# Optimization experiments

Measured on AMD Instinct MI355X. Metric: run time of the kernel, lower is better.

The kernel has to match this reference:

```python
import jax, jax.numpy as jnp
import numpy as np

B, N_PER, DEG = 1024, 256, 16
N = B * N_PER            # 262144 total nodes
E = B * N_PER * DEG      # 4194304 edges
F_IN, H, K, C = 7, 64, 50, 2


def setup_inputs() -> dict:
    key = jax.random.key(0)
    ks = jax.random.split(key, 16)
    rng = np.random.default_rng(0)
    # within-graph random edges: nodes of graph g occupy [g*N_PER, (g+1)*N_PER)
    offs = np.repeat(np.arange(B, dtype=np.int64) * N_PER, N_PER * DEG)
    src = offs + rng.integers(0, N_PER, size=E)
    dst = offs + rng.integers(0, N_PER, size=E)
    edge_index = jnp.asarray(np.stack([src, dst]), dtype=jnp.int64)
    batch = jnp.repeat(jnp.arange(B, dtype=jnp.int64), N_PER)
    sc = lambda fan: 1.0 / np.sqrt(fan)
    return {
        'x': jax.random.normal(ks[0], (N, F_IN), jnp.float32),
        'W1a': jax.random.normal(ks[1], (F_IN, H), jnp.float32) * sc(F_IN),
        'b1a': jnp.zeros((H,), jnp.float32),
        'W1b': jax.random.normal(ks[2], (H, H), jnp.float32) * sc(H),
        'b1b': jnp.zeros((H,), jnp.float32),
        'Wp': jax.random.normal(ks[3], (H, K), jnp.float32) * sc(H),
        'bp': jnp.zeros((K,), jnp.float32),
        'W2a': jax.random.normal(ks[4], (H, H), jnp.float32) * sc(H),
        'b2a': jnp.zeros((H,), jnp.float32),
        'W2b': jax.random.normal(ks[5], (H, H), jnp.float32) * sc(H),
        'b2b': jnp.zeros((H,), jnp.float32),
        'Wl': jax.random.normal(ks[6], (H, C), jnp.float32) * sc(H),
        'bl': jnp.zeros((C,), jnp.float32),
        'edge_index': edge_index,
        'batch': batch,
    }


def reference(x, W1a, b1a, W1b, b1b, Wp, bp, W2a, b2a, W2b, b2b, Wl, bl,
              edge_index, batch):
    src, dst = edge_index[0], edge_index[1]
    # --- sparse GINConv (eps=0): MLP(x + sum_{j in N(i)} x_j) ---
    agg = jnp.zeros_like(x).at[dst].add(x[src])          # scatter-add over edges
    h = jax.nn.relu((x + agg) @ W1a + b1a) @ W1b + b1b   # [N, H]
    # --- densify per graph (equal-size contiguous graphs) ---
    xd = h.reshape(B, N_PER, H)                          # [B, n, H]
    g = src // N_PER
    si = src % N_PER
    di = dst % N_PER
    A = jnp.zeros((B, N_PER, N_PER), x.dtype).at[g, si, di].add(1.0)
    # --- BNPool-style soft cluster pooling ---
    S = jax.nn.softmax(xd @ Wp + bp, axis=-1)            # [B, n, K]
    xp = jnp.einsum('bnk,bnd->bkd', S, xd)               # [B, K, H]
    AS = jnp.einsum('bnm,bmk->bnk', A, S)
    Ap = jnp.einsum('bnk,bnl->bkl', S, AS)               # [B, K, K]
    SSt = jnp.einsum('bnk,bmk->bnm', S, S)
    link_loss = jnp.sqrt(jnp.sum((A - SSt) ** 2)) / A.size
    ent_loss = -jnp.mean(jnp.sum(S * jnp.log(S + 1e-15), axis=-1))
    aux_loss = link_loss + ent_loss
    # --- DenseGINConv (eps=0): MLP(x + A @ x) ---
    h2 = xp + jnp.einsum('bkl,bld->bkd', Ap, xp)
    h2 = jax.nn.relu(h2 @ W2a + b2a) @ W2b + b2b         # [B, K, H]
    # --- mean pool over clusters + classifier ---
    logits = h2.mean(axis=1) @ Wl + bl                   # [B, C]
    return jax.nn.log_softmax(logits, axis=-1), aux_loss
```

## Files before the change

kernel.cpp:

```cpp
#include <hip/hip_runtime.h>
#include <math.h>

#define NG   1024
#define NP   256
#define EPG  4096
#define ETOT 4194304
#define FIN  7
#define HD   64
#define KC   50
#define FST  72
#define TST  264
#define TSC  0.00390625f
#define TSCI 256.0f

#define SW_ST(k, n)  ((k) * 256 + ((n) ^ (((k) & 7) << 3)))
#define SW_AW(r, w)  ((r) * 128 + ((w) ^ (((r) & 7) << 2)))
#define SW_AH(r, h)  ((r) * 256 + ((h) ^ (((r) & 7) << 3)))


typedef __attribute__((ext_vector_type(8))) _Float16 v8h;
typedef __attribute__((ext_vector_type(4))) float v4f;

__device__ __align__(16) _Float16 g_W1bT[HD * HD];
__device__ __align__(16) _Float16 g_WWT[HD * HD];
__device__ __align__(16) _Float16 g_W2aT[HD * HD];
__device__ __align__(16) _Float16 g_W2bT[HD * HD];
__device__ float g_bP[HD];

__global__ void kw_conv(const float* __restrict__ W1b, const float* __restrict__ Wp,
                        const float* __restrict__ W2a, const float* __restrict__ W2b,
                        const float* __restrict__ b1b, const float* __restrict__ bp,
                        float* __restrict__ ws) {
    const int b = blockIdx.x, tid = threadIdx.x;
    if (b == 0 && tid < 4) ws[tid] = 0.f;
    {
        int i = b * 256 + tid;
        int d = i >> 6, j = i & 63;
        g_W1bT[i] = (_Float16)W1b[j * HD + d];
        g_W2aT[i] = (_Float16)W2a[j * HD + d];
        g_W2bT[i] = (_Float16)W2b[j * HD + d];
    }
    {
        int k = b * 4 + (tid >> 6), j = tid & 63;
        float acc = 0.f;
        if (k < KC) {
            for (int d = 0; d < HD; ++d)
                acc += W1b[j * HD + d] * Wp[d * KC + k];
        }
        g_WWT[k * HD + j] = (_Float16)acc;
    }
    if (tid < 4) {
        int k = b * 4 + tid;
        float a = 0.f;
        if (k < KC) {
            for (int d = 0; d < HD; ++d) a += b1b[d] * Wp[d * KC + k];
            a += bp[k];
        }
        g_bP[k] = a;
    }
}

__global__ void finalize_k(const float* __restrict__ ws, float* __restrict__ out) {
    if (threadIdx.x == 0) {
        float num = ws[0] - 2.f * ws[2] + ws[3];
        float link = sqrtf(fmaxf(num, 0.f)) / 67108864.0f;
        float ent  = -ws[1] / 262144.0f;
        out[2048] = link + ent;
    }
}

__device__ __forceinline__ float blockReduceN(float v, float* red, int nw) {
    __syncthreads();
    #pragma unroll
    for (int o = 32; o > 0; o >>= 1) v += __shfl_down(v, o);
    if ((threadIdx.x & 63) == 0) red[threadIdx.x >> 6] = v;
    __syncthreads();
    float r = 0.f;
    if (threadIdx.x == 0) {
        for (int i = 0; i < nw; ++i) r += red[i];
    }
    return r;
}

__device__ __forceinline__ void blockReduce3(float& a, float& b, float& c,
                                             float* red) {
    __syncthreads();
    #pragma unroll
    for (int o = 32; o > 0; o >>= 1) {
        a += __shfl_down(a, o);
        b += __shfl_down(b, o);
        c += __shfl_down(c, o);
    }
    const int wid = threadIdx.x >> 6;
    if ((threadIdx.x & 63) == 0) {
        red[wid * 3] = a; red[wid * 3 + 1] = b; red[wid * 3 + 2] = c;
    }
    __syncthreads();
    if (threadIdx.x == 0) {
        float ra = 0.f, rb = 0.f, rc = 0.f;
        for (int i = 0; i < 16; ++i) {
            ra += red[i * 3]; rb += red[i * 3 + 1]; rc += red[i * 3 + 2];
        }
        a = ra; b = rb; c = rc;
    }
}

__launch_bounds__(1024, 1)
__global__ void mega(const int* __restrict__ esrc, const int* __restrict__ edst,
                     const float* __restrict__ x,
                     const float* __restrict__ W1a, const float* __restrict__ b1a,
                     const float* __restrict__ b1b,
                     const float* __restrict__ b2a, const float* __restrict__ b2b,
                     const float* __restrict__ Wl,  const float* __restrict__ bl,
                     float* __restrict__ out, float* __restrict__ ws)
{
    __shared__ __align__(16) _Float16 ST[64 * 256];
    __shared__ __align__(16) _Float16 xagg[NP * 8];
    __shared__ __align__(16) union {
        struct {
            unsigned char ssi[EPG];
            float xt8[NP * 8];
            unsigned int hist[256], cur[256], roff[NP + 1];
        } k1;
        struct {
            _Float16 t1b[NP * FST];
            _Float16 t1T[HD * TST];
        } k2;
        struct {
            unsigned int cnt[64 * 128];
            _Float16 T1T[64 * FST];
        } a;
        struct {
            _Float16 Apf_tf[64 * FST];
            _Float16 xpT[64 * FST];
            _Float16 h2f[64 * FST];
        } b;
    } u;
    __shared__ float cs[64];
    __shared__ float red[48];

    const int g = blockIdx.x, tid = threadIdx.x;
    const int lane = tid & 63, wid = tid >> 6;
    const int l15 = lane & 15, quad = lane >> 4, fko = quad * 8;
    const int mt = (wid >> 2) << 4, nt = (wid & 3) << 4;

    for (int i = tid; i < 64 * 128; i += 1024) ((unsigned int*)ST)[i] = 0u;
    if (tid < 256) u.k1.hist[tid] = 0u;
    __syncthreads();

    unsigned int cellr[4];
    #pragma unroll
    for (int j = 0; j < 4; ++j) {
        int e = tid + j * 1024;
        int s = esrc[g * EPG + e] & (NP - 1);
        int d = edst[g * EPG + e] & (NP - 1);
        cellr[j] = (unsigned)((s << 8) | d);
        atomicAdd(&u.k1.hist[d], 1u);
    }
    for (int i = tid; i < NP * 8; i += 1024) {
        int n = i >> 3, f = i & 7;
        u.k1.xt8[i] = (f < FIN) ? x[g * NP * FIN + n * FIN + f] : 0.f;
    }
    __syncthreads();

    if (wid == 0) {
        unsigned carry = 0;
        for (int c = 0; c < 4; ++c) {
            unsigned v = u.k1.hist[c * 64 + lane];
            unsigned s = v;
            #pragma unroll
            for (int o = 1; o < 64; o <<= 1) {
                unsigned t = __shfl_up(s, o);
                if (lane >= o) s += t;
            }
            unsigned excl = s - v + carry;
            u.k1.roff[c * 64 + lane] = excl;
            u.k1.cur[c * 64 + lane] = excl;
            carry += __shfl(s, 63);
        }
        if (lane == 0) u.k1.roff[NP] = EPG;
    }
    __syncthreads();

    #pragma unroll
    for (int j = 0; j < 4; ++j) {
        unsigned c = cellr[j];
        unsigned p2 = atomicAdd(&u.k1.cur[c & 255u], 1u);
        u.k1.ssi[p2] = (unsigned char)(c >> 8);
    }
    __syncthreads();

    {
        const int gi = tid >> 3, f = tid & 7;
        for (int n = gi; n < NP; n += 128) {
            int beg = u.k1.roff[n], end = u.k1.roff[n + 1];
            float a = u.k1.xt8[n * 8 + f];
            for (int e = beg; e < end; ++e)
                a += u.k1.xt8[u.k1.ssi[e] * 8 + f];
            xagg[n * 8 + f] = (_Float16)a;
        }
    }
    __syncthreads();

    {
        float w1r[FIN];
        #pragma unroll
        for (int f = 0; f < FIN; ++f) w1r[f] = W1a[f * HD + lane];
        float b1r = b1a[lane];
        for (int it = 0; it < 16; ++it) {
            int n = it * 16 + wid;
            float a = b1r;
            #pragma unroll
            for (int f = 0; f < FIN; ++f)
                a += (float)xagg[n * 8 + f] * w1r[f];
            _Float16 tv = (_Float16)fmaxf(a, 0.f);
            u.k2.t1b[n * FST + lane] = tv;
            u.k2.t1T[lane * TST + n] = tv;
        }
    }
    __syncthreads();

    float entL = 0.f;
    {
        const int r16 = wid << 4;
        v4f pa[4];
        #pragma unroll
        for (int c = 0; c < 4; ++c) {
            v4f acc = {0.f, 0.f, 0.f, 0.f};
            #pragma unroll
            for (int ks = 0; ks < 2; ++ks) {
                v8h af = *(const v8h*)&u.k2.t1b[(r16 + l15) * FST + ks * 32 + fko];
                v8h bf = *(const v8h*)&g_WWT[(c * 16 + l15) * HD + ks * 32 + fko];
                acc = __builtin_amdgcn_mfma_f32_16x16x32_f16(af, bf, acc, 0, 0, 0);
            }
            pa[c] = acc;
        }
        float bv[4]; bool valid[4];
        #pragma unroll
        for (int c = 0; c < 4; ++c) {
            int col = c * 16 + l15;
            bv[c] = g_bP[col];
            valid[c] = col < KC;
        }
        #pragma unroll
        for (int r = 0; r < 4; ++r) {
            float pv[4];
            #pragma unroll
            for (int c = 0; c < 4; ++c)
                pv[c] = valid[c] ? (pa[c][r] + bv[c]) : -INFINITY;
            float m = fmaxf(fmaxf(pv[0], pv[1]), fmaxf(pv[2], pv[3]));
            #pragma unroll
            for (int o = 8; o > 0; o >>= 1) m = fmaxf(m, __shfl_xor(m, o));
            float e[4], Z = 0.f;
            #pragma unroll
            for (int c = 0; c < 4; ++c) {
                e[c] = valid[c] ? __expf(pv[c] - m) : 0.f;
                Z += e[c];
            }
            #pragma unroll
            for (int o = 8; o > 0; o >>= 1) Z += __shfl_xor(Z, o);
            float zi = 1.f / Z, lZ = __logf(Z);
            int row = r16 + quad * 4 + r;
            #pragma unroll
            for (int c = 0; c < 4; ++c) {
                if (valid[c]) {
                    float s = e[c] * zi;
                    ST[SW_ST(c * 16 + l15, row)] = (_Float16)s;
                    entL += s * (pv[c] - m);
                }
            }
            if (l15 == 0) entL -= lZ;
        }
    }
    __syncthreads();

    v4f spa = {0.f, 0.f, 0.f, 0.f};
    {
        const int ar = mt + l15, br = nt + l15;
        #pragma unroll
        for (int ks = 0; ks < 8; ++ks) {
            int ko = ks * 32 + fko;
            v8h af = *(const v8h*)&ST[SW_ST(ar, ko)];
            v8h bf = *(const v8h*)&u.k2.t1T[br * TST + ko];
            spa = __builtin_amdgcn_mfma_f32_16x16x32_f16(af, bf, spa, 0, 0, 0);
        }
    }
    {
        _Float16* SPb = u.k2.t1b;
        int c = nt + l15;
        #pragma unroll
        for (int r = 0; r < 4; ++r)
            SPb[(mt + quad * 4 + r) * FST + c] = (_Float16)spa[r];
    }
    {
        int k = tid >> 4, q = tid & 15;
        float v = 0.f;
        #pragma unroll
        for (int i = 0; i < 16; ++i) v += (float)ST[SW_ST(k, q * 16 + i)];
        #pragma unroll
        for (int o = 8; o > 0; o >>= 1) v += __shfl_xor(v, o);
        if (q == 0) cs[k] = v;
    }
    {
        float rE = blockReduceN(entL, red, 16);
        if (tid == 0) atomicAdd(&ws[1], rE);
    }

    v4f axp;
    {
        const int d = nt + l15;
        float bv = b1b[d];
        #pragma unroll
        for (int r = 0; r < 4; ++r) axp[r] = cs[mt + quad * 4 + r] * bv;
        #pragma unroll
        for (int ks = 0; ks < 2; ++ks) {
            v8h af = *(const v8h*)&u.k2.t1b[(mt + l15) * FST + ks * 32 + fko];
            v8h bf = *(const v8h*)&g_W1bT[(nt + l15) * HD + ks * 32 + fko];
            axp = __builtin_amdgcn_mfma_f32_16x16x32_f16(af, bf, axp, 0, 0, 0);
        }
    }
    __syncthreads();

    float sumA2 = 0.f;
    v4f ap = {0.f, 0.f, 0.f, 0.f};
    v4f ag = {0.f, 0.f, 0.f, 0.f};

    for (int ch = 0; ch < 4; ++ch) {
        for (int i = tid; i < 64 * 128; i += 1024) u.a.cnt[i] = 0u;
        __syncthreads();

        int rlo = ch << 6;
        #pragma unroll
        for (int j = 0; j < 4; ++j) {
            unsigned c = cellr[j];
            int sr = (int)(c >> 8) - rlo;
            if ((unsigned)sr < 64u) {
                int d = c & 255u;
                atomicAdd(&u.a.cnt[SW_AW(sr, d >> 1)],
                          (d & 1) ? 0x10000u : 1u);
            }
        }
        __syncthreads();

        for (int i = tid; i < 64 * 128; i += 1024) {
            unsigned v = u.a.cnt[i];
            float m0 = (float)(v & 0xffffu), m1 = (float)(v >> 16);
            sumA2 += m0 * m0 + m1 * m1;
            union { unsigned uu; _Float16 h[2]; } cv;
            cv.h[0] = (_Float16)m0; cv.h[1] = (_Float16)m1;
            u.a.cnt[i] = cv.uu;
        }
        __syncthreads();

        const _Float16* Af = (const _Float16*)u.a.cnt;

        {
            const int ar = mt + l15, br = nt + l15;
            v4f acc = {0.f, 0.f, 0.f, 0.f};
            #pragma unroll
            for (int ks = 0; ks < 8; ++ks) {
                v8h af = *(const v8h*)&Af[SW_AH(ar, ks * 32 + fko)];
                v8h bf = *(const v8h*)&ST[SW_ST(br, ks * 32 + fko)];
                acc = __builtin_amdgcn_mfma_f32_16x16x32_f16(af, bf, acc, 0, 0, 0);
            }
            int c = nt + l15;
            #pragma unroll
            for (int r = 0; r < 4; ++r)
                u.a.T1T[c * FST + mt + quad * 4 + r] = (_Float16)acc[r];
        }
        __syncthreads();

        {
            const int ar = mt + l15, br = nt + l15;
            #pragma unroll
            for (int ks = 0; ks < 2; ++ks) {
                int ko = (ch << 6) + ks * 32 + fko;
                v8h af = *(const v8h*)&ST[SW_ST(ar, ko)];
                v8h bt = *(const v8h*)&u.a.T1T[br * FST + ks * 32 + fko];
                v8h bs = *(const v8h*)&ST[SW_ST(br, ko)];
                ap = __builtin_amdgcn_mfma_f32_16x16x32_f16(af, bt, ap, 0, 0, 0);
                ag = __builtin_amdgcn_mfma_f32_16x16x32_f16(af, bs, ag, 0, 0, 0);
            }
        }
        __syncthreads();
    }

    float tr = 0.f, g2 = 0.f;
    {
        int c = nt + l15;
        #pragma unroll
        for (int r = 0; r < 4; ++r) {
            int k = mt + quad * 4 + r;
            u.b.Apf_tf[k * FST + c] = (_Float16)ap[r];
            u.b.xpT[c * FST + k] = (_Float16)axp[r];
            if (k < KC && c < KC) {
                if (k == c) tr += ap[r];
                g2 += ag[r] * ag[r];
            }
        }
    }

    blockReduce3(sumA2, tr, g2, red);
    if (tid == 0) {
        atomicAdd(&ws[0], sumA2);
        atomicAdd(&ws[2], tr);
        atomicAdd(&ws[3], g2);
    }
    __syncthreads();

    {
        v4f hacc = axp;
        #pragma unroll
        for (int ks = 0; ks < 2; ++ks) {
            v8h af = *(const v8h*)&u.b.Apf_tf[(mt + l15) * FST + ks * 32 + fko];
            v8h bf = *(const v8h*)&u.b.xpT[(nt + l15) * FST + ks * 32 + fko];
            hacc = __builtin_amdgcn_mfma_f32_16x16x32_f16(af, bf, hacc, 0, 0, 0);
        }
        int d = nt + l15;
        #pragma unroll
        for (int r = 0; r < 4; ++r)
            u.b.h2f[(mt + quad * 4 + r) * FST + d] = (_Float16)(hacc[r] * TSC);
    }
    __syncthreads();

    {
        float bv = b2a[nt + l15] * TSC;
        v4f tacc = {bv, bv, bv, bv};
        #pragma unroll
        for (int ks = 0; ks < 2; ++ks) {
            v8h af = *(const v8h*)&u.b.h2f[(mt + l15) * FST + ks * 32 + fko];
            v8h bf = *(const v8h*)&g_W2aT[(nt + l15) * 64 + ks * 32 + fko];
            tacc = __builtin_amdgcn_mfma_f32_16x16x32_f16(af, bf, tacc, 0, 0, 0);
        }
        int d2 = nt + l15;
        #pragma unroll
        for (int r = 0; r < 4; ++r)
            u.b.Apf_tf[(mt + quad * 4 + r) * FST + d2] = (_Float16)fmaxf(tacc[r], 0.f);
    }
    __syncthreads();

    float l0 = 0.f, l1 = 0.f;
    {
        v4f oacc = {0.f, 0.f, 0.f, 0.f};
        #pragma unroll
        for (int ks = 0; ks < 2; ++ks) {
            v8h af = *(const v8h*)&u.b.Apf_tf[(mt + l15) * FST + ks * 32 + fko];
            v8h bf = *(const v8h*)&g_W2bT[(nt + l15) * 64 + ks * 32 + fko];
            oacc = __builtin_amdgcn_mfma_f32_16x16x32_f16(af, bf, oacc, 0, 0, 0);
        }
        int j = nt + l15;
        float bv = b2b[j];
        float wl0 = Wl[j * 2], wl1 = Wl[j * 2 + 1];
        #pragma unroll
        for (int r = 0; r < 4; ++r) {
            int k = mt + quad * 4 + r;
            if (k < KC) {
                float h3v = oacc[r] * TSCI + bv;
                l0 += h3v * wl0; l1 += h3v * wl1;
            }
        }
    }

    float dummy = 0.f;
    blockReduce3(l0, l1, dummy, red);
    if (tid == 0) {
        float g0 = bl[0] + l0 * (1.f / KC);
        float g1 = bl[1] + l1 * (1.f / KC);
        float mm = fmaxf(g0, g1);
        float lse = mm + logf(expf(g0 - mm) + expf(g1 - mm));
        out[2 * g]     = g0 - lse;
        out[2 * g + 1] = g1 - lse;
    }
}

extern "C" void kernel_launch(void* const* d_in, const int* in_sizes, int n_in,
                              void* d_out, int out_size, void* d_ws, size_t ws_size,
                              hipStream_t stream) {
    const float* x    = (const float*)d_in[0];
    const float* W1a  = (const float*)d_in[1];
    const float* b1a  = (const float*)d_in[2];
    const float* W1b  = (const float*)d_in[3];
    const float* b1b  = (const float*)d_in[4];
    const float* Wp   = (const float*)d_in[5];
    const float* bp   = (const float*)d_in[6];
    const float* W2a  = (const float*)d_in[7];
    const float* b2a  = (const float*)d_in[8];
    const float* W2b  = (const float*)d_in[9];
    const float* b2b  = (const float*)d_in[10];
    const float* Wl   = (const float*)d_in[11];
    const float* bl   = (const float*)d_in[12];
    const int*   eidx = (const int*)d_in[13];
    float* out = (float*)d_out;
    float* ws  = (float*)d_ws;

    kw_conv<<<16, 256, 0, stream>>>(W1b, Wp, W2a, W2b, b1b, bp, ws);
    mega<<<NG, 1024, 0, stream>>>(eidx, eidx + ETOT, x,
                                  W1a, b1a, b1b,
                                  b2a, b2b, Wl, bl, out, ws);
    finalize_k<<<1, 64, 0, stream>>>(ws, out);
}
```

Measured before the change: 254.8 us.

## Halve block size and shrink shared memory to fit multiple blocks per CU

The fused per-graph kernel moves from 1024 to 512 threads per block with launch bounds allowing 4 blocks per CU. Shared-memory footprint is reduced by processing the node MLP in two 128-node halves, dropping the transposed t1 buffer, and halving the adjacency count tile so the A·S product runs in 8 chunks of 32 rows. Each wave now owns two output tiles, and the entropy reduction is merged into the final block reduction. The intent is higher occupancy and overlap across graphs, at the cost of more chunks, extra barriers and more register pressure per thread.

```diff
diff --git a/kernel.cpp b/kernel.cpp
--- a/kernel.cpp
+++ b/kernel.cpp
@@ -9,7 +9,7 @@
 #define HD   64
 #define KC   50
 #define FST  72
-#define TST  264
+#define FT2  68
 #define TSC  0.00390625f
 #define TSCI 256.0f
 
@@ -29,10 +29,8 @@
 
 __global__ void kw_conv(const float* __restrict__ W1b, const float* __restrict__ Wp,
                         const float* __restrict__ W2a, const float* __restrict__ W2b,
-                        const float* __restrict__ b1b, const float* __restrict__ bp,
-                        float* __restrict__ ws) {
+                        const float* __restrict__ b1b, const float* __restrict__ bp) {
     const int b = blockIdx.x, tid = threadIdx.x;
-    if (b == 0 && tid < 4) ws[tid] = 0.f;
     {
         int i = b * 256 + tid;
         int d = i >> 6, j = i & 63;
@@ -69,21 +67,8 @@
     }
 }
 
-__device__ __forceinline__ float blockReduceN(float v, float* red, int nw) {
-    __syncthreads();
-    #pragma unroll
-    for (int o = 32; o > 0; o >>= 1) v += __shfl_down(v, o);
-    if ((threadIdx.x & 63) == 0) red[threadIdx.x >> 6] = v;
-    __syncthreads();
-    float r = 0.f;
-    if (threadIdx.x == 0) {
-        for (int i = 0; i < nw; ++i) r += red[i];
-    }
-    return r;
-}
-
-__device__ __forceinline__ void blockReduce3(float& a, float& b, float& c,
-                                             float* red) {
+__device__ __forceinline__ void blockReduce3w8(float& a, float& b, float& c,
+                                               float* red) {
     __syncthreads();
     #pragma unroll
     for (int o = 32; o > 0; o >>= 1) {
@@ -98,14 +83,14 @@
     __syncthreads();
     if (threadIdx.x == 0) {
         float ra = 0.f, rb = 0.f, rc = 0.f;
-        for (int i = 0; i < 16; ++i) {
+        for (int i = 0; i < 8; ++i) {
             ra += red[i * 3]; rb += red[i * 3 + 1]; rc += red[i * 3 + 2];
         }
         a = ra; b = rb; c = rc;
     }
 }
 
-__launch_bounds__(1024, 1)
+__launch_bounds__(512, 4)
 __global__ void mega(const int* __restrict__ esrc, const int* __restrict__ edst,
                      const float* __restrict__ x,
                      const float* __restrict__ W1a, const float* __restrict__ b1a,
@@ -123,41 +108,39 @@
             unsigned int hist[256], cur[256], roff[NP + 1];
         } k1;
         struct {
-            _Float16 t1b[NP * FST];
-            _Float16 t1T[HD * TST];
+            _Float16 t1b[128 * FST];
         } k2;
         struct {
-            unsigned int cnt[64 * 128];
-            _Float16 T1T[64 * FST];
+            unsigned int cnt[32 * 128];
+            _Float16 ast[64 * 36];
         } a;
         struct {
-            _Float16 Apf_tf[64 * FST];
-            _Float16 xpT[64 * FST];
-            _Float16 h2f[64 * FST];
+            _Float16 Apf_tf[64 * FT2];
+            _Float16 xpT[64 * FT2];
+            _Float16 h2f[64 * FT2];
         } b;
     } u;
     __shared__ float cs[64];
-    __shared__ float red[48];
+    __shared__ float red[24];
 
     const int g = blockIdx.x, tid = threadIdx.x;
     const int lane = tid & 63, wid = tid >> 6;
     const int l15 = lane & 15, quad = lane >> 4, fko = quad * 8;
-    const int mt = (wid >> 2) << 4, nt = (wid & 3) << 4;
-
-    for (int i = tid; i < 64 * 128; i += 1024) ((unsigned int*)ST)[i] = 0u;
+
+    for (int i = tid; i < 64 * 128; i += 512) ((unsigned int*)ST)[i] = 0u;
     if (tid < 256) u.k1.hist[tid] = 0u;
     __syncthreads();
 
-    unsigned int cellr[4];
-    #pragma unroll
-    for (int j = 0; j < 4; ++j) {
-        int e = tid + j * 1024;
+    unsigned int cellr[8];
+    #pragma unroll
+    for (int j = 0; j < 8; ++j) {
+        int e = tid + j * 512;
         int s = esrc[g * EPG + e] & (NP - 1);
         int d = edst[g * EPG + e] & (NP - 1);
         cellr[j] = (unsigned)((s << 8) | d);
         atomicAdd(&u.k1.hist[d], 1u);
     }
-    for (int i = tid; i < NP * 8; i += 1024) {
+    for (int i = tid; i < NP * 8; i += 512) {
         int n = i >> 3, f = i & 7;
         u.k1.xt8[i] = (f < FIN) ? x[g * NP * FIN + n * FIN + f] : 0.f;
     }
@@ -183,7 +166,7 @@
     __syncthreads();
 
     #pragma unroll
-    for (int j = 0; j < 4; ++j) {
+    for (int j = 0; j < 8; ++j) {
         unsigned c = cellr[j];
         unsigned p2 = atomicAdd(&u.k1.cur[c & 255u], 1u);
         u.k1.ssi[p2] = (unsigned char)(c >> 8);
@@ -192,7 +175,7 @@
 
     {
         const int gi = tid >> 3, f = tid & 7;
-        for (int n = gi; n < NP; n += 128) {
+        for (int n = gi; n < NP; n += 64) {
             int beg = u.k1.roff[n], end = u.k1.roff[n + 1];
             float a = u.k1.xt8[n * 8 + f];
             for (int e = beg; e < end; ++e)
@@ -202,152 +185,171 @@
     }
     __syncthreads();
 
+    float entL = 0.f;
+    v8h a0, a1, a2, a3;
     {
         float w1r[FIN];
         #pragma unroll
         for (int f = 0; f < FIN; ++f) w1r[f] = W1a[f * HD + lane];
         float b1r = b1a[lane];
-        for (int it = 0; it < 16; ++it) {
-            int n = it * 16 + wid;
-            float a = b1r;
-            #pragma unroll
-            for (int f = 0; f < FIN; ++f)
-                a += (float)xagg[n * 8 + f] * w1r[f];
-            _Float16 tv = (_Float16)fmaxf(a, 0.f);
-            u.k2.t1b[n * FST + lane] = tv;
-            u.k2.t1T[lane * TST + n] = tv;
-        }
-    }
-    __syncthreads();
-
-    float entL = 0.f;
+
+        #pragma unroll
+        for (int h = 0; h < 2; ++h) {
+            for (int it = 0; it < 16; ++it) {
+                int n = it * 8 + wid;
+                float a = b1r;
+                #pragma unroll
+                for (int f = 0; f < FIN; ++f)
+                    a += (float)xagg[(h * 128 + n) * 8 + f] * w1r[f];
+                u.k2.t1b[n * FST + lane] = (_Float16)fmaxf(a, 0.f);
+            }
+            __syncthreads();
+
+            v8h f0 = *(const v8h*)&u.k2.t1b[(wid * 16 + l15) * FST + fko];
+            v8h f1 = *(const v8h*)&u.k2.t1b[(wid * 16 + l15) * FST + 32 + fko];
+            if (h == 0) { a0 = f0; a1 = f1; } else { a2 = f0; a3 = f1; }
+
+            v4f pa[4];
+            #pragma unroll
+            for (int c2 = 0; c2 < 4; ++c2) {
+                v4f acc = {0.f, 0.f, 0.f, 0.f};
+                v8h bf0 = *(const v8h*)&g_WWT[(c2 * 16 + l15) * HD + fko];
+                v8h bf1 = *(const v8h*)&g_WWT[(c2 * 16 + l15) * HD + 32 + fko];
+                acc = __builtin_amdgcn_mfma_f32_16x16x32_f16(f0, bf0, acc, 0, 0, 0);
+                acc = __builtin_amdgcn_mfma_f32_16x16x32_f16(f1, bf1, acc, 0, 0, 0);
+                pa[c2] = acc;
+            }
+            float bv[4]; bool valid[4];
+            #pragma unroll
+            for (int c2 = 0; c2 < 4; ++c2) {
+                int col = c2 * 16 + l15;
+                bv[c2] = g_bP[col];
+                valid[c2] = col < KC;
+            }
+            #pragma unroll
+            for (int r = 0; r < 4; ++r) {
+                float pv[4];
+                #pragma unroll
+                for (int c2 = 0; c2 < 4; ++c2)
+                    pv[c2] = valid[c2] ? (pa[c2][r] + bv[c2]) : -INFINITY;
+                float m = fmaxf(fmaxf(pv[0], pv[1]), fmaxf(pv[2], pv[3]));
+                #pragma unroll
+                for (int o = 8; o > 0; o >>= 1) m = fmaxf(m, __shfl_xor(m, o));
+                float e[4], Z = 0.f;
+                #pragma unroll
+                for (int c2 = 0; c2 < 4; ++c2) {
+                    e[c2] = valid[c2] ? __expf(pv[c2] - m) : 0.f;
+                    Z += e[c2];
+                }
+                #pragma unroll
+                for (int o = 8; o > 0; o >>= 1) Z += __shfl_xor(Z, o);
+                float zi = 1.f / Z, lZ = __logf(Z);
+                int row = h * 128 + wid * 16 + quad * 4 + r;
+                #pragma unroll
+                for (int c2 = 0; c2 < 4; ++c2) {
+                    if (valid[c2]) {
+                        float s = e[c2] * zi;
+                        ST[SW_ST(c2 * 16 + l15, row)] = (_Float16)s;
+                        entL += s * (pv[c2] - m);
+                    }
+                }
+                if (l15 == 0) entL -= lZ;
+            }
+            __syncthreads();
+        }
+    }
+
     {
-        const int r16 = wid << 4;
-        v4f pa[4];
-        #pragma unroll
-        for (int c = 0; c < 4; ++c) {
-            v4f acc = {0.f, 0.f, 0.f, 0.f};
+        int k = tid >> 3, q = tid & 7;
+        float v = 0.f;
+        #pragma unroll
+        for (int i = 0; i < 32; ++i) v += (float)ST[SW_ST(k, q * 32 + i)];
+        #pragma unroll
+        for (int o = 4; o > 0; o >>= 1) v += __shfl_xor(v, o);
+        if (q == 0) cs[k] = v;
+    }
+
+    v4f spa[2] = {{0.f, 0.f, 0.f, 0.f}, {0.f, 0.f, 0.f, 0.f}};
+    #pragma unroll
+    for (int c = 0; c < 4; ++c) {
+        if ((wid >> 2) == (c & 1)) {
+            int nl = (wid & 3) * 16 + l15;
+            v8h t0 = (c >> 1) ? a2 : a0;
+            v8h t1v = (c >> 1) ? a3 : a1;
+            #pragma unroll
+            for (int k = 0; k < 8; ++k) {
+                u.k2.t1b[(fko + k) * FST + nl] = t0[k];
+                u.k2.t1b[(32 + fko + k) * FST + nl] = t1v[k];
+            }
+        }
+        __syncthreads();
+        #pragma unroll
+        for (int tt = 0; tt < 2; ++tt) {
+            int t = wid * 2 + tt;
+            int mtt = (t >> 2) << 4, ntt = (t & 3) << 4;
             #pragma unroll
             for (int ks = 0; ks < 2; ++ks) {
-                v8h af = *(const v8h*)&u.k2.t1b[(r16 + l15) * FST + ks * 32 + fko];
-                v8h bf = *(const v8h*)&g_WWT[(c * 16 + l15) * HD + ks * 32 + fko];
-                acc = __builtin_amdgcn_mfma_f32_16x16x32_f16(af, bf, acc, 0, 0, 0);
-            }
-            pa[c] = acc;
-        }
-        float bv[4]; bool valid[4];
-        #pragma unroll
-        for (int c = 0; c < 4; ++c) {
-            int col = c * 16 + l15;
-            bv[c] = g_bP[col];
-            valid[c] = col < KC;
-        }
-        #pragma unroll
-        for (int r = 0; r < 4; ++r) {
-            float pv[4];
-            #pragma unroll
-            for (int c = 0; c < 4; ++c)
-                pv[c] = valid[c] ? (pa[c][r] + bv[c]) : -INFINITY;
-            float m = fmaxf(fmaxf(pv[0], pv[1]), fmaxf(pv[2], pv[3]));
-            #pragma unroll
-            for (int o = 8; o > 0; o >>= 1) m = fmaxf(m, __shfl_xor(m, o));
-            float e[4], Z = 0.f;
-            #pragma unroll
-            for (int c = 0; c < 4; ++c) {
-                e[c] = valid[c] ? __expf(pv[c] - m) : 0.f;
-                Z += e[c];
-            }
-            #pragma unroll
-            for (int o = 8; o > 0; o >>= 1) Z += __shfl_xor(Z, o);
-            float zi = 1.f / Z, lZ = __logf(Z);
-            int row = r16 + quad * 4 + r;
-            #pragma unroll
-            for (int c = 0; c < 4; ++c) {
-                if (valid[c]) {
-                    float s = e[c] * zi;
-                    ST[SW_ST(c * 16 + l15, row)] = (_Float16)s;
-                    entL += s * (pv[c] - m);
-                }
-            }
-            if (l15 == 0) entL -= lZ;
-        }
-    }
-    __syncthreads();
-
-    v4f spa = {0.f, 0.f, 0.f, 0.f};
-    {
-        const int ar = mt + l15, br = nt + l15;
-        #pragma unroll
-        for (int ks = 0; ks < 8; ++ks) {
-            int ko = ks * 32 + fko;
-            v8h af = *(const v8h*)&ST[SW_ST(ar, ko)];
-            v8h bf = *(const v8h*)&u.k2.t1T[br * TST + ko];
-            spa = __builtin_amdgcn_mfma_f32_16x16x32_f16(af, bf, spa, 0, 0, 0);
-        }
-    }
-    {
-        _Float16* SPb = u.k2.t1b;
-        int c = nt + l15;
+                v8h af = *(const v8h*)&ST[SW_ST(mtt + l15, c * 64 + ks * 32 + fko)];
+                v8h bf = *(const v8h*)&u.k2.t1b[(ntt + l15) * FST + ks * 32 + fko];
+                spa[tt] = __builtin_amdgcn_mfma_f32_16x16x32_f16(af, bf, spa[tt], 0, 0, 0);
+            }
+        }
+        __syncthreads();
+    }
+
+    #pragma unroll
+    for (int tt = 0; tt < 2; ++tt) {
+        int t = wid * 2 + tt;
+        int mtt = (t >> 2) << 4, ntt = (t & 3) << 4;
         #pragma unroll
         for (int r = 0; r < 4; ++r)
-            SPb[(mt + quad * 4 + r) * FST + c] = (_Float16)spa[r];
-    }
-    {
-        int k = tid >> 4, q = tid & 15;
-        float v = 0.f;
-        #pragma unroll
-        for (int i = 0; i < 16; ++i) v += (float)ST[SW_ST(k, q * 16 + i)];
-        #pragma unroll
-        for (int o = 8; o > 0; o >>= 1) v += __shfl_xor(v, o);
-        if (q == 0) cs[k] = v;
-    }
-    {
-        float rE = blockReduceN(entL, red, 16);
-        if (tid == 0) atomicAdd(&ws[1], rE);
-    }
-
-    v4f axp;
-    {
-        const int d = nt + l15;
-        float bv = b1b[d];
-        #pragma unroll
-        for (int r = 0; r < 4; ++r) axp[r] = cs[mt + quad * 4 + r] * bv;
+            u.k2.t1b[(mtt + quad * 4 + r) * FST + ntt + l15] = (_Float16)spa[tt][r];
+    }
+    __syncthreads();
+
+    v4f axp[2];
+    #pragma unroll
+    for (int tt = 0; tt < 2; ++tt) {
+        int t = wid * 2 + tt;
+        int mtt = (t >> 2) << 4, ntt = (t & 3) << 4;
+        float bv = b1b[ntt + l15];
+        #pragma unroll
+        for (int r = 0; r < 4; ++r) axp[tt][r] = cs[mtt + quad * 4 + r] * bv;
         #pragma unroll
         for (int ks = 0; ks < 2; ++ks) {
-            v8h af = *(const v8h*)&u.k2.t1b[(mt + l15) * FST + ks * 32 + fko];
-            v8h bf = *(const v8h*)&g_W1bT[(nt + l15) * HD + ks * 32 + fko];
-            axp = __builtin_amdgcn_mfma_f32_16x16x32_f16(af, bf, axp, 0, 0, 0);
+            v8h af = *(const v8h*)&u.k2.t1b[(mtt + l15) * FST + ks * 32 + fko];
+            v8h bf = *(const v8h*)&g_W1bT[(ntt + l15) * HD + ks * 32 + fko];
+            axp[tt] = __builtin_amdgcn_mfma_f32_16x16x32_f16(af, bf, axp[tt], 0, 0, 0);
         }
     }
     __syncthreads();
 
     float sumA2 = 0.f;
-    v4f ap = {0.f, 0.f, 0.f, 0.f};
-    v4f ag = {0.f, 0.f, 0.f, 0.f};
-
-    for (int ch = 0; ch < 4; ++ch) {
-        for (int i = tid; i < 64 * 128; i += 1024) u.a.cnt[i] = 0u;
-        __syncthreads();
-
-        int rlo = ch << 6;
-        #pragma unroll
-        for (int j = 0; j < 4; ++j) {
+    v4f ap[2] = {{0.f, 0.f, 0.f, 0.f}, {0.f, 0.f, 0.f, 0.f}};
+    v4f ag[2] = {{0.f, 0.f, 0.f, 0.f}, {0.f, 0.f, 0.f, 0.f}};
+
+    for (int i = tid; i < 32 * 128; i += 512) u.a.cnt[i] = 0u;
+    __syncthreads();
+
+    for (int ch = 0; ch < 8; ++ch) {
+        int rlo = ch << 5;
+        #pragma unroll
+        for (int j = 0; j < 8; ++j) {
             unsigned c = cellr[j];
             int sr = (int)(c >> 8) - rlo;
-            if ((unsigned)sr < 64u) {
+            if ((unsigned)sr < 32u) {
                 int d = c & 255u;
-                atomicAdd(&u.a.cnt[SW_AW(sr, d >> 1)],
-                          (d & 1) ? 0x10000u : 1u);
+                atomicAdd(&u.a.cnt[SW_AW(sr, d >> 1)], (d & 1) ? 0x10000u : 1u);
             }
         }
         __syncthreads();
 
-        for (int i = tid; i < 64 * 128; i += 1024) {
+        for (int i = tid; i < 32 * 128; i += 512) {
             unsigned v = u.a.cnt[i];
             float m0 = (float)(v & 0xffffu), m1 = (float)(v >> 16);
             sumA2 += m0 * m0 + m1 * m1;
-            union { unsigned uu; _Float16 h[2]; } cv;
-            cv.h[0] = (_Float16)m0; cv.h[1] = (_Float16)m1;
+            union { unsigned uu; _Float16 hh[2]; } cv;
+            cv.hh[0] = (_Float16)m0; cv.hh[1] = (_Float16)m1;
             u.a.cnt[i] = cv.uu;
         }
         __syncthreads();
@@ -355,52 +357,55 @@
         const _Float16* Af = (const _Float16*)u.a.cnt;
 
         {
-            const int ar = mt + l15, br = nt + l15;
+            int mt3 = (wid >> 2) << 4, nt3 = (wid & 3) << 4;
             v4f acc = {0.f, 0.f, 0.f, 0.f};
             #pragma unroll
             for (int ks = 0; ks < 8; ++ks) {
-                v8h af = *(const v8h*)&Af[SW_AH(ar, ks * 32 + fko)];
-                v8h bf = *(const v8h*)&ST[SW_ST(br, ks * 32 + fko)];
+                v8h af = *(const v8h*)&Af[SW_AH(mt3 + l15, ks * 32 + fko)];
+                v8h bf = *(const v8h*)&ST[SW_ST(nt3 + l15, ks * 32 + fko)];
                 acc = __builtin_amdgcn_mfma_f32_16x16x32_f16(af, bf, acc, 0, 0, 0);
             }
-            int c = nt + l15;
             #pragma unroll
             for (int r = 0; r < 4; ++r)
-                u.a.T1T[c * FST + mt + quad * 4 + r] = (_Float16)acc[r];
+                u.a.ast[(nt3 + l15) * 36 + mt3 + quad * 4 + r] = (_Float16)acc[r];
         }
         __syncthreads();
 
-        {
-            const int ar = mt + l15, br = nt + l15;
-            #pragma unroll
-            for (int ks = 0; ks < 2; ++ks) {
-                int ko = (ch << 6) + ks * 32 + fko;
-                v8h af = *(const v8h*)&ST[SW_ST(ar, ko)];
-                v8h bt = *(const v8h*)&u.a.T1T[br * FST + ks * 32 + fko];
-                v8h bs = *(const v8h*)&ST[SW_ST(br, ko)];
-                ap = __builtin_amdgcn_mfma_f32_16x16x32_f16(af, bt, ap, 0, 0, 0);
-                ag = __builtin_amdgcn_mfma_f32_16x16x32_f16(af, bs, ag, 0, 0, 0);
-            }
+        #pragma unroll
+        for (int tt = 0; tt < 2; ++tt) {
+            int t = wid * 2 + tt;
+            int mtt = (t >> 2) << 4, ntt = (t & 3) << 4;
+            v8h af = *(const v8h*)&ST[SW_ST(mtt + l15, (ch << 5) + fko)];
+            v8h bt = *(const v8h*)&u.a.ast[(ntt + l15) * 36 + fko];
+            v8h bs = *(const v8h*)&ST[SW_ST(ntt + l15, (ch << 5) + fko)];
+            ap[tt] = __builtin_amdgcn_mfma_f32_16x16x32_f16(af, bt, ap[tt], 0, 0, 0);
+            ag[tt] = __builtin_amdgcn_mfma_f32_16x16x32_f16(af, bs, ag[tt], 0, 0, 0);
+        }
+        if (ch < 7) {
+            for (int i = tid; i < 32 * 128; i += 512) u.a.cnt[i] = 0u;
         }
         __syncthreads();
     }
 
     float tr = 0.f, g2 = 0.f;
-    {
-        int c = nt + l15;
+    #pragma unroll
+    for (int tt = 0; tt < 2; ++tt) {
+        int t = wid * 2 + tt;
+        int mtt = (t >> 2) << 4, ntt = (t & 3) << 4;
+        int c = ntt + l15;
         #pragma unroll
         for (int r = 0; r < 4; ++r) {
-            int k = mt + quad * 4 + r;
-            u.b.Apf_tf[k * FST + c] = (_Float16)ap[r];
-            u.b.xpT[c * FST + k] = (_Float16)axp[r];
+            int k = mtt + quad * 4 + r;
+            u.b.Apf_tf[k * FT2 + c] = (_Float16)ap[tt][r];
+            u.b.xpT[c * FT2 + k] = (_Float16)axp[tt][r];
             if (k < KC && c < KC) {
-                if (k == c) tr += ap[r];
-                g2 += ag[r] * ag[r];
-            }
-        }
-    }
-
-    blockReduce3(sumA2, tr, g2, red);
+                if (k == c) tr += ap[tt][r];
+                g2 += ag[tt][r] * ag[tt][r];
+            }
+        }
+    }
+
+    blockReduce3w8(sumA2, tr, g2, red);
     if (tid == 0) {
         atomicAdd(&ws[0], sumA2);
         atomicAdd(&ws[2], tr);
@@ -408,52 +413,59 @@
     }
     __syncthreads();
 
-    {
-        v4f hacc = axp;
+    #pragma unroll
+    for (int tt = 0; tt < 2; ++tt) {
+        int t = wid * 2 + tt;
+        int mtt = (t >> 2) << 4, ntt = (t & 3) << 4;
+        v4f hacc = axp[tt];
         #pragma unroll
         for (int ks = 0; ks < 2; ++ks) {
-            v8h af = *(const v8h*)&u.b.Apf_tf[(mt + l15) * FST + ks * 32 + fko];
-            v8h bf = *(const v8h*)&u.b.xpT[(nt + l15) * FST + ks * 32 + fko];
+            v8h af = *(const v8h*)&u.b.Apf_tf[(mtt + l15) * FT2 + ks * 32 + fko];
+            v8h bf = *(const v8h*)&u.b.xpT[(ntt + l15) * FT2 + ks * 32 + fko];
             hacc = __builtin_amdgcn_mfma_f32_16x16x32_f16(af, bf, hacc, 0, 0, 0);
         }
-        int d = nt + l15;
         #pragma unroll
         for (int r = 0; r < 4; ++r)
-            u.b.h2f[(mt + quad * 4 + r) * FST + d] = (_Float16)(hacc[r] * TSC);
-    }
-    __syncthreads();
-
-    {
-        float bv = b2a[nt + l15] * TSC;
+            u.b.h2f[(mtt + quad * 4 + r) * FT2 + ntt + l15] = (_Float16)(hacc[r] * TSC);
+    }
+    __syncthreads();
+
+    #pragma unroll
+    for (int tt = 0; tt < 2; ++tt) {
+        int t = wid * 2 + tt;
+        int mtt = (t >> 2) << 4, ntt = (t & 3) << 4;
+        float bv = b2a[ntt + l15] * TSC;
         v4f tacc = {bv, bv, bv, bv};
         #pragma unroll
         for (int ks = 0; ks < 2; ++ks) {
-            v8h af = *(const v8h*)&u.b.h2f[(mt + l15) * FST + ks * 32 + fko];
-            v8h bf = *(const v8h*)&g_W2aT[(nt + l15) * 64 + ks * 32 + fko];
+            v8h af = *(const v8h*)&u.b.h2f[(mtt + l15) * FT2 + ks * 32 + fko];
+            v8h bf = *(const v8h*)&g_W2aT[(ntt + l15) * HD + ks * 32 + fko];
             tacc = __builtin_amdgcn_mfma_f32_16x16x32_f16(af, bf, tacc, 0, 0, 0);
         }
-        int d2 = nt + l15;
         #pragma unroll
         for (int r = 0; r < 4; ++r)
-            u.b.Apf_tf[(mt + quad * 4 + r) * FST + d2] = (_Float16)fmaxf(tacc[r], 0.f);
+            u.b.Apf_tf[(mtt + quad * 4 + r) * FT2 + ntt + l15] = (_Float16)fmaxf(tacc[r], 0.f);
     }
     __syncthreads();
 
     float l0 = 0.f, l1 = 0.f;
-    {
+    #pragma unroll
+    for (int tt = 0; tt < 2; ++tt) {
+        int t = wid * 2 + tt;
+        int mtt = (t >> 2) << 4, ntt = (t & 3) << 4;
         v4f oacc = {0.f, 0.f, 0.f, 0.f};
         #pragma unroll
         for (int ks = 0; ks < 2; ++ks) {
-            v8h af = *(const v8h*)&u.b.Apf_tf[(mt + l15) * FST + ks * 32 + fko];
-            v8h bf = *(const v8h*)&g_W2bT[(nt + l15) * 64 + ks * 32 + fko];
+            v8h af = *(const v8h*)&u.b.Apf_tf[(mtt + l15) * FT2 + ks * 32 + fko];
+            v8h bf = *(const v8h*)&g_W2bT[(ntt + l15) * HD + ks * 32 + fko];
             oacc = __builtin_amdgcn_mfma_f32_16x16x32_f16(af, bf, oacc, 0, 0, 0);
         }
-        int j = nt + l15;
+        int j = ntt + l15;
         float bv = b2b[j];
         float wl0 = Wl[j * 2], wl1 = Wl[j * 2 + 1];
         #pragma unroll
         for (int r = 0; r < 4; ++r) {
-            int k = mt + quad * 4 + r;
+            int k = mtt + quad * 4 + r;
             if (k < KC) {
                 float h3v = oacc[r] * TSCI + bv;
                 l0 += h3v * wl0; l1 += h3v * wl1;
@@ -461,13 +473,13 @@
         }
     }
 
-    float dummy = 0.f;
-    blockReduce3(l0, l1, dummy, red);
+    blockReduce3w8(l0, l1, entL, red);
     if (tid == 0) {
+        atomicAdd(&ws[1], entL);
         float g0 = bl[0] + l0 * (1.f / KC);
         float g1 = bl[1] + l1 * (1.f / KC);
         float mm = fmaxf(g0, g1);
-        float lse = mm + logf(expf(g0 - mm) + expf(g1 - mm));
+        float lse = mm + __logf(__expf(g0 - mm) + __expf(g1 - mm));
         out[2 * g]     = g0 - lse;
         out[2 * g + 1] = g1 - lse;
     }
@@ -493,9 +505,10 @@
     float* out = (float*)d_out;
     float* ws  = (float*)d_ws;
 
-    kw_conv<<<16, 256, 0, stream>>>(W1b, Wp, W2a, W2b, b1b, bp, ws);
-    mega<<<NG, 1024, 0, stream>>>(eidx, eidx + ETOT, x,
-                                  W1a, b1a, b1b,
-                                  b2a, b2b, Wl, bl, out, ws);
+    hipMemsetAsync(ws, 0, 4 * sizeof(float), stream);
+    kw_conv<<<16, 256, 0, stream>>>(W1b, Wp, W2a, W2b, b1b, bp);
+    mega<<<NG, 512, 0, stream>>>(eidx, eidx + ETOT, x,
+                                 W1a, b1a, b1b,
+                                 b2a, b2b, Wl, bl, out, ws);
     finalize_k<<<1, 64, 0, stream>>>(ws, out);
 }
```

After: 238.0 us. 6.6% less time.
